# Kernel tuning notes

Measured on AMD Instinct MI355X. Metric: run time of the kernel, lower is better.

## Reference

```python
import jax, jax.numpy as jnp
import numpy as np

N_USERS, N_ITEMS = 40000, 60000
N = N_USERS + N_ITEMS
N_EDGES = 600000
IN_DIM, HID, OUT = 128, 256, 256


def setup_inputs() -> dict:
    key = jax.random.key(0)
    ks = jax.random.split(key, 8)
    return {
        "user_feat": jax.random.normal(ks[0], (N_USERS, IN_DIM), jnp.float32),
        "item_feat": jax.random.normal(ks[1], (N_ITEMS, IN_DIM), jnp.float32),
        "edge_rows": jax.random.randint(ks[2], (N_EDGES,), 0, N, jnp.int32),
        "edge_cols": jax.random.randint(ks[3], (N_EDGES,), 0, N, jnp.int32),
        "edge_vals": jax.random.uniform(ks[4], (N_EDGES,), jnp.float32),
        "W0": jax.random.normal(ks[5], (IN_DIM, HID), jnp.float32) * (1.0 / np.sqrt(IN_DIM)),
        "b0": jnp.zeros((HID,), jnp.float32),
        "Wres0": jax.random.normal(ks[6], (IN_DIM, HID), jnp.float32) * (1.0 / np.sqrt(IN_DIM)),
        "W1": jax.random.normal(ks[7], (HID, OUT), jnp.float32) * (1.0 / np.sqrt(HID)),
        "b1": jnp.zeros((OUT,), jnp.float32),
    }


def reference(user_feat, item_feat, edge_rows, edge_cols, edge_vals, W0, b0, Wres0, W1, b1):
    n_users = user_feat.shape[0]
    n_total = n_users + item_feat.shape[0]

    def spmm(x):  # sparse adjacency @ dense features via gather + segment-sum
        return jax.ops.segment_sum(edge_vals[:, None] * x[edge_cols], edge_rows,
                                   num_segments=n_total)

    # Layer 0: fc -> SpMM -> linear residual -> relu (norm=None, dropout eval no-op)
    x = jnp.concatenate([user_feat @ W0 + b0, item_feat @ W0 + b0])  # [N, HID]
    h = spmm(x)
    res = jnp.concatenate([user_feat, item_feat]) @ Wres0  # in_dim != out_dim -> Linear residual
    h = jax.nn.relu(h + res)

    # Layer 1 (last, encoding=False): fc -> SpMM, no residual/norm/activation
    x = h @ W1 + b1
    h = spmm(x)

    return h[:n_users], h[n_users:]
```

## Files before the change

### kernel.cpp

```cpp
#include <hip/hip_runtime.h>

#define N_USERS 40000
#define N_ITEMS 60000
#define N_TOTAL 100000
#define M_PAD   100032
#define NEDGES  600000
#define IN_DIM  128
#define HID     256

typedef short  bf16x8 __attribute__((ext_vector_type(8)));
typedef float  f32x4  __attribute__((ext_vector_type(4)));
typedef unsigned short ushort4v __attribute__((ext_vector_type(4)));
typedef unsigned short ushort8v __attribute__((ext_vector_type(8)));

__device__ __forceinline__ unsigned short f2bf(float f) {
    unsigned u = __builtin_bit_cast(unsigned, f);
    unsigned r = (u + 0x7FFFu + ((u >> 16) & 1u)) >> 16;
    return (unsigned short)r;
}
__device__ __forceinline__ float bf2f(unsigned short b) {
    unsigned u = ((unsigned)b) << 16;
    return __builtin_bit_cast(float, u);
}

__device__ __forceinline__ void gload_lds16(const void* g, void* l) {
    __builtin_amdgcn_global_load_lds(
        (const __attribute__((address_space(1))) unsigned int*)g,
        (__attribute__((address_space(3))) unsigned int*)l, 16, 0, 0);
}

__global__ __launch_bounds__(256) void prep_feats(const float* __restrict__ uf,
                                                  const float* __restrict__ itf,
                                                  unsigned short* __restrict__ outp) {
    const long i8 = (long)(blockIdx.x * 256 + threadIdx.x) * 8;
    if (i8 >= (long)N_TOTAL * IN_DIM) return;
    const long uend = (long)N_USERS * IN_DIM;
    const float4* src = (i8 < uend) ? (const float4*)(uf + i8)
                                    : (const float4*)(itf + (i8 - uend));
    float4 a = src[0], b = src[1];
    ushort8v o;
    o[0] = f2bf(a.x); o[1] = f2bf(a.y); o[2] = f2bf(a.z); o[3] = f2bf(a.w);
    o[4] = f2bf(b.x); o[5] = f2bf(b.y); o[6] = f2bf(b.z); o[7] = f2bf(b.w);
    *(ushort8v*)(outp + i8) = o;
}

__global__ __launch_bounds__(256) void prep_weights(const float* __restrict__ W0,
                                                    const float* __restrict__ Wres0,
                                                    const float* __restrict__ W1,
                                                    unsigned short* __restrict__ Wcat_t,
                                                    unsigned short* __restrict__ W1_t) {
    const int id = blockIdx.x * 256 + threadIdx.x;
    if (id < 512 * IN_DIM) {
        const int n = id >> 7, k = id & 127;
        const float v = (n < HID) ? W0[(size_t)k * HID + n]
                                  : Wres0[(size_t)k * HID + (n - HID)];
        Wcat_t[id] = f2bf(v);
    } else {
        const int id2 = id - 512 * IN_DIM;
        const int n = id2 >> 8, k = id2 & 255;
        W1_t[id2] = f2bf(W1[(size_t)k * HID + n]);
    }
}

template <int K>
__device__ __forceinline__ void stageB(const unsigned short* __restrict__ Bg,
                                       char* bs, int kk, int t) {
    #pragma unroll
    for (int i = 0; i < 4; ++i) {
        const int L = (i * 256 + t) * 16;
        const int n = L >> 6;
        const int q = (L >> 4) & 3;
        gload_lds16((const char*)(Bg + (size_t)n * K + kk + q * 8), bs + L);
    }
}

template <int K, int EPI>
__global__ __launch_bounds__(256) void mfma_gemm2(const unsigned short* __restrict__ A,
                                                  const unsigned short* __restrict__ Bt,
                                                  const float* __restrict__ bias,
                                                  unsigned short* __restrict__ out0,
                                                  unsigned short* __restrict__ out1) {
    constexpr int NK    = K / 32;
    constexpr int SHIFT = (K == 256) ? 9 : 8;
    __shared__ unsigned short As[64 * K];
    __shared__ unsigned short Bs[2][256 * 32];

    const int t  = threadIdx.x;
    const int w  = t >> 6, l = t & 63;
    const int fr = l & 15, fb = l >> 4;
    const int wr = w >> 1, wc = w & 1;
    const int m0 = blockIdx.x * 64;
    const int gy = blockIdx.y;

    const char* Ag = (const char*)(A + (size_t)m0 * K);
    constexpr int ACALLS = (64 * K * 2) / (16 * 256);
    #pragma unroll
    for (int i = 0; i < ACALLS; ++i) {
        const int L = (i * 256 + t) * 16;
        const int U = L ^ (((L >> SHIFT) & 7) << 4);
        gload_lds16(Ag + U, (char*)As + L);
    }
    const unsigned short* Bg = Bt + (size_t)gy * 256 * K;
    stageB<K>(Bg, (char*)Bs[0], 0, t);
    __syncthreads();

    f32x4 acc[2][8] = {};
    for (int kt = 0; kt < NK; ++kt) {
        if (kt + 1 < NK) stageB<K>(Bg, (char*)Bs[(kt + 1) & 1], (kt + 1) * 32, t);

        const char* as_base = (const char*)As;
        const char* bs_base = (const char*)Bs[kt & 1];
        bf16x8 af[2];
        #pragma unroll
        for (int rb = 0; rb < 2; ++rb) {
            const int row = wr * 32 + rb * 16 + fr;
            const int Sa = ((row * K + kt * 32 + fb * 8) * 2) ^ ((fr & 7) << 4);
            af[rb] = *(const bf16x8*)(as_base + Sa);
        }
        #pragma unroll
        for (int nt = 0; nt < 8; ++nt) {
            const int Sb = ((wc * 128 + nt * 16 + fr) * 32 + fb * 8) * 2;
            const bf16x8 bfr = *(const bf16x8*)(bs_base + Sb);
            acc[0][nt] = __builtin_amdgcn_mfma_f32_16x16x32_bf16(af[0], bfr, acc[0][nt], 0, 0, 0);
            acc[1][nt] = __builtin_amdgcn_mfma_f32_16x16x32_bf16(af[1], bfr, acc[1][nt], 0, 0, 0);
        }
        __syncthreads();
    }

    const bool use1 = (EPI == 1) && (gy == 1);
    unsigned short* outp = use1 ? out1 : out0;
    #pragma unroll
    for (int rb = 0; rb < 2; ++rb) {
        #pragma unroll
        for (int nt = 0; nt < 8; ++nt) {
            const int col = wc * 128 + nt * 16 + fr;
            const float bv = use1 ? 0.f : bias[col];
            #pragma unroll
            for (int j = 0; j < 4; ++j) {
                const int row = m0 + wr * 32 + rb * 16 + fb * 4 + j;
                if (row < N_TOTAL)
                    outp[(size_t)row * HID + col] = f2bf(acc[rb][nt][j] + bv);
            }
        }
    }
}

__global__ __launch_bounds__(256) void edge_histogram(const int* __restrict__ rows,
                                                      int* __restrict__ cnt) {
    int e = blockIdx.x * 256 + threadIdx.x;
    if (e < NEDGES) atomicAdd(&cnt[rows[e]], 1);
}

#define SCAN_B 1024
__global__ __launch_bounds__(SCAN_B) void scan_blocks(const int* __restrict__ cnt,
                                                      int* __restrict__ row_ptr,
                                                      int* __restrict__ bsums) {
    __shared__ int s[SCAN_B];
    const int gid = blockIdx.x * SCAN_B + threadIdx.x;
    const int v = (gid < N_TOTAL) ? cnt[gid] : 0;
    s[threadIdx.x] = v;
    __syncthreads();
    for (int off = 1; off < SCAN_B; off <<= 1) {
        int tv = (threadIdx.x >= off) ? s[threadIdx.x - off] : 0;
        __syncthreads();
        s[threadIdx.x] += tv;
        __syncthreads();
    }
    if (gid < N_TOTAL) row_ptr[gid] = s[threadIdx.x] - v;
    if (threadIdx.x == SCAN_B - 1) bsums[blockIdx.x] = s[threadIdx.x];
}

__global__ __launch_bounds__(128) void scan_sums(int* __restrict__ bsums, int nb) {
    __shared__ int s[128];
    const int v = (threadIdx.x < nb) ? bsums[threadIdx.x] : 0;
    s[threadIdx.x] = v;
    __syncthreads();
    for (int off = 1; off < 128; off <<= 1) {
        int tv = (threadIdx.x >= off) ? s[threadIdx.x - off] : 0;
        __syncthreads();
        s[threadIdx.x] += tv;
        __syncthreads();
    }
    if (threadIdx.x < nb) bsums[threadIdx.x] = s[threadIdx.x] - v;
}

__global__ __launch_bounds__(SCAN_B) void scan_apply(int* __restrict__ row_ptr,
                                                     const int* __restrict__ bsums,
                                                     int* __restrict__ next) {
    const int gid = blockIdx.x * SCAN_B + threadIdx.x;
    if (gid < N_TOTAL) {
        const int p = row_ptr[gid] + bsums[blockIdx.x];
        row_ptr[gid] = p;
        next[gid] = p;
    }
    if (gid == 0) row_ptr[N_TOTAL] = NEDGES;
}

__global__ __launch_bounds__(256) void csr_fill(const int* __restrict__ rows,
                                                const int* __restrict__ cols,
                                                const float* __restrict__ vals,
                                                int* __restrict__ next,
                                                int2* __restrict__ cvp) {
    int e = blockIdx.x * 256 + threadIdx.x;
    if (e >= NEDGES) return;
    const int slot = atomicAdd(&next[rows[e]], 1);
    int2 p;
    p.x = cols[e];
    p.y = __builtin_bit_cast(int, vals[e]);
    cvp[slot] = p;
}

template <bool FUSE>
__global__ __launch_bounds__(256) void spmm_bf16(const int* __restrict__ row_ptr,
                                                 const int2* __restrict__ cvp,
                                                 const unsigned short* __restrict__ X,
                                                 unsigned short* __restrict__ Ybf,
                                                 float* __restrict__ Yf) {
    const int wid  = (blockIdx.x * 256 + threadIdx.x) >> 6;
    const int lane = threadIdx.x & 63;
    if (wid >= N_TOTAL) return;
    const int beg = row_ptr[wid], end = row_ptr[wid + 1];

    float a0 = 0.f, a1 = 0.f, a2 = 0.f, a3 = 0.f;
    int e = beg;
    for (; e + 1 < end; e += 2) {
        const int2 p0 = cvp[e], p1 = cvp[e + 1];
        const float v0 = __builtin_bit_cast(float, p0.y);
        const float v1 = __builtin_bit_cast(float, p1.y);
        const ushort4v x0 = *(const ushort4v*)(X + (size_t)p0.x * HID + lane * 4);
        const ushort4v x1 = *(const ushort4v*)(X + (size_t)p1.x * HID + lane * 4);
        a0 = fmaf(v0, bf2f(x0[0]), a0); a1 = fmaf(v0, bf2f(x0[1]), a1);
        a2 = fmaf(v0, bf2f(x0[2]), a2); a3 = fmaf(v0, bf2f(x0[3]), a3);
        a0 = fmaf(v1, bf2f(x1[0]), a0); a1 = fmaf(v1, bf2f(x1[1]), a1);
        a2 = fmaf(v1, bf2f(x1[2]), a2); a3 = fmaf(v1, bf2f(x1[3]), a3);
    }
    if (e < end) {
        const int2 p0 = cvp[e];
        const float v0 = __builtin_bit_cast(float, p0.y);
        const ushort4v x0 = *(const ushort4v*)(X + (size_t)p0.x * HID + lane * 4);
        a0 = fmaf(v0, bf2f(x0[0]), a0); a1 = fmaf(v0, bf2f(x0[1]), a1);
        a2 = fmaf(v0, bf2f(x0[2]), a2); a3 = fmaf(v0, bf2f(x0[3]), a3);
    }

    if (FUSE) {
        unsigned short* yp = Ybf + (size_t)wid * HID + lane * 4;
        const ushort4v rv = *(const ushort4v*)yp;
        a0 = fmaxf(a0 + bf2f(rv[0]), 0.f);
        a1 = fmaxf(a1 + bf2f(rv[1]), 0.f);
        a2 = fmaxf(a2 + bf2f(rv[2]), 0.f);
        a3 = fmaxf(a3 + bf2f(rv[3]), 0.f);
        ushort4v o; o[0] = f2bf(a0); o[1] = f2bf(a1); o[2] = f2bf(a2); o[3] = f2bf(a3);
        *(ushort4v*)yp = o;
    } else {
        f32x4 o = {a0, a1, a2, a3};
        *(f32x4*)(Yf + (size_t)wid * HID + lane * 4) = o;
    }
}

extern "C" void kernel_launch(void* const* d_in, const int* in_sizes, int n_in,
                              void* d_out, int out_size, void* d_ws, size_t ws_size,
                              hipStream_t stream) {
    const float* user_feat = (const float*)d_in[0];
    const float* item_feat = (const float*)d_in[1];
    const int*   edge_rows = (const int*)d_in[2];
    const int*   edge_cols = (const int*)d_in[3];
    const float* edge_vals = (const float*)d_in[4];
    const float* W0    = (const float*)d_in[5];
    const float* b0    = (const float*)d_in[6];
    const float* Wres0 = (const float*)d_in[7];
    const float* W1    = (const float*)d_in[8];
    const float* b1    = (const float*)d_in[9];
    float* out = (float*)d_out;

    char* ws = (char*)d_ws;
    auto take = [&](size_t bytes) { char* p = ws; ws += (bytes + 255) & ~(size_t)255; return p; };
    unsigned short* x      = (unsigned short*)take((size_t)M_PAD * HID * 2);
    unsigned short* h      = (unsigned short*)take((size_t)M_PAD * HID * 2);
    unsigned short* feats  = (unsigned short*)take((size_t)M_PAD * IN_DIM * 2);
    unsigned short* Wcat_t = (unsigned short*)take(512 * IN_DIM * 2);
    unsigned short* W1_t   = (unsigned short*)take(HID * HID * 2);
    int*   row_ptr = (int*)take((N_TOTAL + 1) * 4);
    int*   cnt     = (int*)take(N_TOTAL * 4);
    int*   nxt     = (int*)take(N_TOTAL * 4);
    int*   bsums   = (int*)take(128 * 4);
    int2*  cvp     = (int2*)take((size_t)NEDGES * 8);

    const dim3 blk(256);
    const int nscan = (N_TOTAL + SCAN_B - 1) / SCAN_B;

    prep_feats<<<(N_TOTAL * IN_DIM / 8 + 255) / 256, blk, 0, stream>>>(user_feat, item_feat, feats);
    prep_weights<<<(512 * IN_DIM + HID * HID) / 256, blk, 0, stream>>>(W0, Wres0, W1, Wcat_t, W1_t);

    hipMemsetAsync(cnt, 0, N_TOTAL * 4, stream);
    edge_histogram<<<(NEDGES + 255) / 256, blk, 0, stream>>>(edge_rows, cnt);
    scan_blocks<<<nscan, SCAN_B, 0, stream>>>(cnt, row_ptr, bsums);
    scan_sums<<<1, 128, 0, stream>>>(bsums, nscan);
    scan_apply<<<nscan, SCAN_B, 0, stream>>>(row_ptr, bsums, nxt);
    csr_fill<<<(NEDGES + 255) / 256, blk, 0, stream>>>(edge_rows, edge_cols, edge_vals,
                                                       nxt, cvp);

    mfma_gemm2<IN_DIM, 1><<<dim3(M_PAD / 64, 2), blk, 0, stream>>>(feats, Wcat_t, b0, x, h);

    const int spmm_blocks = (N_TOTAL * 64 + 255) / 256;
    spmm_bf16<true><<<spmm_blocks, blk, 0, stream>>>(row_ptr, cvp, x, h, nullptr);

    mfma_gemm2<HID, 0><<<dim3(M_PAD / 64, 1), blk, 0, stream>>>(h, W1_t, b1, x, nullptr);

    spmm_bf16<false><<<spmm_blocks, blk, 0, stream>>>(row_ptr, cvp, x, nullptr, out);
}
```

Before: 458.5 us.

## Reassociate layer-0 SpMM before the fc and fuse the residual into one GEMM

Uses A(XW0+b0) = (AX)W0 + rowsum(A)·b0, so the first SpMM aggregates the 128-wide bf16 input features instead of the 256-wide hidden ones. It also returns per-row weight sums. A single K=256 GEMM over the concatenated [AX, X] against stacked [W0; Wres0] then computes the hidden layer, adds the scaled bias and applies ReLU in its epilogue. This removes the separate residual read-modify-write pass. The GEMM epilogue now stages its tile in LDS so it can write coalesced 16-byte global stores. The cost is an extra LDS round trip and a barrier per block, plus some extra rounding from storing AX in bf16.

Measured after the change: 422.0 us. 1.09x faster.

```diff
diff --git a/kernel.cpp b/kernel.cpp
--- a/kernel.cpp
+++ b/kernel.cpp
@@ -47,79 +47,84 @@
 __global__ __launch_bounds__(256) void prep_weights(const float* __restrict__ W0,
                                                     const float* __restrict__ Wres0,
                                                     const float* __restrict__ W1,
-                                                    unsigned short* __restrict__ Wcat_t,
+                                                    unsigned short* __restrict__ Wcat2_t,
                                                     unsigned short* __restrict__ W1_t) {
     const int id = blockIdx.x * 256 + threadIdx.x;
-    if (id < 512 * IN_DIM) {
-        const int n = id >> 7, k = id & 127;
-        const float v = (n < HID) ? W0[(size_t)k * HID + n]
-                                  : Wres0[(size_t)k * HID + (n - HID)];
-        Wcat_t[id] = f2bf(v);
+    if (id < HID * HID) {
+        const int n = id >> 8, k = id & 255;
+        const float v = (k < IN_DIM) ? W0[(size_t)k * HID + n]
+                                     : Wres0[(size_t)(k - IN_DIM) * HID + n];
+        Wcat2_t[id] = f2bf(v);
     } else {
-        const int id2 = id - 512 * IN_DIM;
+        const int id2 = id - HID * HID;
         const int n = id2 >> 8, k = id2 & 255;
         W1_t[id2] = f2bf(W1[(size_t)k * HID + n]);
     }
 }
 
-template <int K>
-__device__ __forceinline__ void stageB(const unsigned short* __restrict__ Bg,
-                                       char* bs, int kk, int t) {
+template <int EPI, bool DUAL>
+__global__ __launch_bounds__(256) void mfma_gemm4(const unsigned short* __restrict__ A0,
+                                                  const unsigned short* __restrict__ A1,
+                                                  const unsigned short* __restrict__ Bt,
+                                                  const float* __restrict__ bias,
+                                                  const float* __restrict__ dscale,
+                                                  unsigned short* __restrict__ outp) {
+    __shared__ unsigned short As[64 * 256];
+    __shared__ unsigned short Bs[2][256 * 32];
+
+    const int t  = threadIdx.x;
+    const int w  = t >> 6, l = t & 63;
+    const int fr = l & 15, fb = l >> 4;
+    const int wr = w >> 1, wc = w & 1;
+    const int m0 = blockIdx.x * 64;
+
+    #pragma unroll
+    for (int i = 0; i < 8; ++i) {
+        const int L   = (i * 256 + t) * 16;
+        const int row = L >> 9;
+        const int W   = L & 511;
+        const int U   = W ^ ((row & 7) << 4);
+        const char* src;
+        if (DUAL) {
+            src = (U < 256) ? (const char*)A0 + (size_t)(m0 + row) * 256 + U
+                            : (const char*)A1 + (size_t)(m0 + row) * 256 + (U - 256);
+        } else {
+            src = (const char*)A0 + (size_t)(m0 + row) * 512 + U;
+        }
+        gload_lds16(src, (char*)As + L);
+    }
     #pragma unroll
     for (int i = 0; i < 4; ++i) {
         const int L = (i * 256 + t) * 16;
         const int n = L >> 6;
         const int q = (L >> 4) & 3;
-        gload_lds16((const char*)(Bg + (size_t)n * K + kk + q * 8), bs + L);
-    }
-}
-
-template <int K, int EPI>
-__global__ __launch_bounds__(256) void mfma_gemm2(const unsigned short* __restrict__ A,
-                                                  const unsigned short* __restrict__ Bt,
-                                                  const float* __restrict__ bias,
-                                                  unsigned short* __restrict__ out0,
-                                                  unsigned short* __restrict__ out1) {
-    constexpr int NK    = K / 32;
-    constexpr int SHIFT = (K == 256) ? 9 : 8;
-    __shared__ unsigned short As[64 * K];
-    __shared__ unsigned short Bs[2][256 * 32];
-
-    const int t  = threadIdx.x;
-    const int w  = t >> 6, l = t & 63;
-    const int fr = l & 15, fb = l >> 4;
-    const int wr = w >> 1, wc = w & 1;
-    const int m0 = blockIdx.x * 64;
-    const int gy = blockIdx.y;
-
-    const char* Ag = (const char*)(A + (size_t)m0 * K);
-    constexpr int ACALLS = (64 * K * 2) / (16 * 256);
-    #pragma unroll
-    for (int i = 0; i < ACALLS; ++i) {
-        const int L = (i * 256 + t) * 16;
-        const int U = L ^ (((L >> SHIFT) & 7) << 4);
-        gload_lds16(Ag + U, (char*)As + L);
-    }
-    const unsigned short* Bg = Bt + (size_t)gy * 256 * K;
-    stageB<K>(Bg, (char*)Bs[0], 0, t);
+        gload_lds16((const char*)Bt + (size_t)n * 512 + q * 16, (char*)Bs[0] + L);
+    }
     __syncthreads();
 
     f32x4 acc[2][8] = {};
-    for (int kt = 0; kt < NK; ++kt) {
-        if (kt + 1 < NK) stageB<K>(Bg, (char*)Bs[(kt + 1) & 1], (kt + 1) * 32, t);
-
-        const char* as_base = (const char*)As;
-        const char* bs_base = (const char*)Bs[kt & 1];
+    for (int kt = 0; kt < 8; ++kt) {
+        if (kt < 7) {
+            #pragma unroll
+            for (int i = 0; i < 4; ++i) {
+                const int L = (i * 256 + t) * 16;
+                const int n = L >> 6;
+                const int q = (L >> 4) & 3;
+                gload_lds16((const char*)Bt + (size_t)n * 512 + (kt + 1) * 64 + q * 16,
+                            (char*)Bs[(kt + 1) & 1] + L);
+            }
+        }
         bf16x8 af[2];
         #pragma unroll
         for (int rb = 0; rb < 2; ++rb) {
             const int row = wr * 32 + rb * 16 + fr;
-            const int Sa = ((row * K + kt * 32 + fb * 8) * 2) ^ ((fr & 7) << 4);
-            af[rb] = *(const bf16x8*)(as_base + Sa);
-        }
+            const int Sa  = (row * 512 + kt * 64 + fb * 16) ^ ((fr & 7) << 4);
+            af[rb] = *(const bf16x8*)((const char*)As + Sa);
+        }
+        const char* bs_base = (const char*)Bs[kt & 1];
         #pragma unroll
         for (int nt = 0; nt < 8; ++nt) {
-            const int Sb = ((wc * 128 + nt * 16 + fr) * 32 + fb * 8) * 2;
+            const int Sb = (wc * 128 + nt * 16 + fr) * 64 + fb * 16;
             const bf16x8 bfr = *(const bf16x8*)(bs_base + Sb);
             acc[0][nt] = __builtin_amdgcn_mfma_f32_16x16x32_bf16(af[0], bfr, acc[0][nt], 0, 0, 0);
             acc[1][nt] = __builtin_amdgcn_mfma_f32_16x16x32_bf16(af[1], bfr, acc[1][nt], 0, 0, 0);
@@ -127,22 +132,30 @@
         __syncthreads();
     }
 
-    const bool use1 = (EPI == 1) && (gy == 1);
-    unsigned short* outp = use1 ? out1 : out0;
+    unsigned short* Hb = As;
     #pragma unroll
     for (int rb = 0; rb < 2; ++rb) {
         #pragma unroll
-        for (int nt = 0; nt < 8; ++nt) {
-            const int col = wc * 128 + nt * 16 + fr;
-            const float bv = use1 ? 0.f : bias[col];
+        for (int j = 0; j < 4; ++j) {
+            const int rl = wr * 32 + rb * 16 + fb * 4 + j;
+            const float ds = (EPI == 1) ? dscale[m0 + rl] : 0.f;
             #pragma unroll
-            for (int j = 0; j < 4; ++j) {
-                const int row = m0 + wr * 32 + rb * 16 + fb * 4 + j;
-                if (row < N_TOTAL)
-                    outp[(size_t)row * HID + col] = f2bf(acc[rb][nt][j] + bv);
+            for (int nt = 0; nt < 8; ++nt) {
+                const int col = wc * 128 + nt * 16 + fr;
+                float v = acc[rb][nt][j];
+                if (EPI == 1) v = fmaxf(v + ds * bias[col], 0.f);
+                else          v = v + bias[col];
+                Hb[rl * 256 + col] = f2bf(v);
             }
         }
     }
+    __syncthreads();
+    const int rowl = t >> 2;
+    const int cb   = (t & 3) * 64;
+    unsigned short* gp = outp + (size_t)(m0 + rowl) * HID + cb;
+    #pragma unroll
+    for (int i = 0; i < 8; ++i)
+        *(ushort8v*)(gp + i * 8) = *(const ushort8v*)(Hb + rowl * 256 + cb + i * 8);
 }
 
 __global__ __launch_bounds__(256) void edge_histogram(const int* __restrict__ rows,
@@ -210,12 +223,47 @@
     cvp[slot] = p;
 }
 
-template <bool FUSE>
-__global__ __launch_bounds__(256) void spmm_bf16(const int* __restrict__ row_ptr,
+__global__ __launch_bounds__(256) void spmm_feat(const int* __restrict__ row_ptr,
                                                  const int2* __restrict__ cvp,
-                                                 const unsigned short* __restrict__ X,
-                                                 unsigned short* __restrict__ Ybf,
-                                                 float* __restrict__ Yf) {
+                                                 const unsigned short* __restrict__ F,
+                                                 unsigned short* __restrict__ G,
+                                                 float* __restrict__ D) {
+    const int wid  = (blockIdx.x * 256 + threadIdx.x) >> 6;
+    const int lane = threadIdx.x & 63;
+    if (wid >= N_TOTAL) return;
+    const int beg = row_ptr[wid], end = row_ptr[wid + 1];
+
+    float a0 = 0.f, a1 = 0.f, ds = 0.f;
+    int e = beg;
+    for (; e + 1 < end; e += 2) {
+        const int2 p0 = cvp[e], p1 = cvp[e + 1];
+        const float v0 = __builtin_bit_cast(float, p0.y);
+        const float v1 = __builtin_bit_cast(float, p1.y);
+        ds += v0 + v1;
+        const unsigned x0 = *(const unsigned*)(F + (size_t)p0.x * IN_DIM + lane * 2);
+        const unsigned x1 = *(const unsigned*)(F + (size_t)p1.x * IN_DIM + lane * 2);
+        a0 = fmaf(v0, bf2f((unsigned short)(x0 & 0xFFFF)), a0);
+        a1 = fmaf(v0, bf2f((unsigned short)(x0 >> 16)),   a1);
+        a0 = fmaf(v1, bf2f((unsigned short)(x1 & 0xFFFF)), a0);
+        a1 = fmaf(v1, bf2f((unsigned short)(x1 >> 16)),   a1);
+    }
+    if (e < end) {
+        const int2 p0 = cvp[e];
+        const float v0 = __builtin_bit_cast(float, p0.y);
+        ds += v0;
+        const unsigned x0 = *(const unsigned*)(F + (size_t)p0.x * IN_DIM + lane * 2);
+        a0 = fmaf(v0, bf2f((unsigned short)(x0 & 0xFFFF)), a0);
+        a1 = fmaf(v0, bf2f((unsigned short)(x0 >> 16)),   a1);
+    }
+    const unsigned ov = (unsigned)f2bf(a0) | ((unsigned)f2bf(a1) << 16);
+    *(unsigned*)(G + (size_t)wid * IN_DIM + lane * 2) = ov;
+    if (lane == 0) D[wid] = ds;
+}
+
+__global__ __launch_bounds__(256) void spmm_out(const int* __restrict__ row_ptr,
+                                                const int2* __restrict__ cvp,
+                                                const unsigned short* __restrict__ X,
+                                                float* __restrict__ Yf) {
     const int wid  = (blockIdx.x * 256 + threadIdx.x) >> 6;
     const int lane = threadIdx.x & 63;
     if (wid >= N_TOTAL) return;
@@ -241,20 +289,8 @@
         a0 = fmaf(v0, bf2f(x0[0]), a0); a1 = fmaf(v0, bf2f(x0[1]), a1);
         a2 = fmaf(v0, bf2f(x0[2]), a2); a3 = fmaf(v0, bf2f(x0[3]), a3);
     }
-
-    if (FUSE) {
-        unsigned short* yp = Ybf + (size_t)wid * HID + lane * 4;
-        const ushort4v rv = *(const ushort4v*)yp;
-        a0 = fmaxf(a0 + bf2f(rv[0]), 0.f);
-        a1 = fmaxf(a1 + bf2f(rv[1]), 0.f);
-        a2 = fmaxf(a2 + bf2f(rv[2]), 0.f);
-        a3 = fmaxf(a3 + bf2f(rv[3]), 0.f);
-        ushort4v o; o[0] = f2bf(a0); o[1] = f2bf(a1); o[2] = f2bf(a2); o[3] = f2bf(a3);
-        *(ushort4v*)yp = o;
-    } else {
-        f32x4 o = {a0, a1, a2, a3};
-        *(f32x4*)(Yf + (size_t)wid * HID + lane * 4) = o;
-    }
+    f32x4 o = {a0, a1, a2, a3};
+    *(f32x4*)(Yf + (size_t)wid * HID + lane * 4) = o;
 }
 
 extern "C" void kernel_launch(void* const* d_in, const int* in_sizes, int n_in,
@@ -274,11 +310,13 @@
 
     char* ws = (char*)d_ws;
     auto take = [&](size_t bytes) { char* p = ws; ws += (bytes + 255) & ~(size_t)255; return p; };
-    unsigned short* x      = (unsigned short*)take((size_t)M_PAD * HID * 2);
-    unsigned short* h      = (unsigned short*)take((size_t)M_PAD * HID * 2);
-    unsigned short* feats  = (unsigned short*)take((size_t)M_PAD * IN_DIM * 2);
-    unsigned short* Wcat_t = (unsigned short*)take(512 * IN_DIM * 2);
-    unsigned short* W1_t   = (unsigned short*)take(HID * HID * 2);
+    unsigned short* feats   = (unsigned short*)take((size_t)M_PAD * IN_DIM * 2);
+    unsigned short* g       = (unsigned short*)take((size_t)M_PAD * IN_DIM * 2);
+    unsigned short* h       = (unsigned short*)take((size_t)M_PAD * HID * 2);
+    unsigned short* x2      = (unsigned short*)take((size_t)M_PAD * HID * 2);
+    float*          d       = (float*)take((size_t)M_PAD * 4);
+    unsigned short* Wcat2_t = (unsigned short*)take(HID * HID * 2);
+    unsigned short* W1_t    = (unsigned short*)take(HID * HID * 2);
     int*   row_ptr = (int*)take((N_TOTAL + 1) * 4);
     int*   cnt     = (int*)take(N_TOTAL * 4);
     int*   nxt     = (int*)take(N_TOTAL * 4);
@@ -289,7 +327,7 @@
     const int nscan = (N_TOTAL + SCAN_B - 1) / SCAN_B;
 
     prep_feats<<<(N_TOTAL * IN_DIM / 8 + 255) / 256, blk, 0, stream>>>(user_feat, item_feat, feats);
-    prep_weights<<<(512 * IN_DIM + HID * HID) / 256, blk, 0, stream>>>(W0, Wres0, W1, Wcat_t, W1_t);
+    prep_weights<<<(2 * HID * HID) / 256, blk, 0, stream>>>(W0, Wres0, W1, Wcat2_t, W1_t);
 
     hipMemsetAsync(cnt, 0, N_TOTAL * 4, stream);
     edge_histogram<<<(NEDGES + 255) / 256, blk, 0, stream>>>(edge_rows, cnt);
@@ -299,12 +337,13 @@
     csr_fill<<<(NEDGES + 255) / 256, blk, 0, stream>>>(edge_rows, edge_cols, edge_vals,
                                                        nxt, cvp);
 
-    mfma_gemm2<IN_DIM, 1><<<dim3(M_PAD / 64, 2), blk, 0, stream>>>(feats, Wcat_t, b0, x, h);
-
     const int spmm_blocks = (N_TOTAL * 64 + 255) / 256;
-    spmm_bf16<true><<<spmm_blocks, blk, 0, stream>>>(row_ptr, cvp, x, h, nullptr);
-
-    mfma_gemm2<HID, 0><<<dim3(M_PAD / 64, 1), blk, 0, stream>>>(h, W1_t, b1, x, nullptr);
-
-    spmm_bf16<false><<<spmm_blocks, blk, 0, stream>>>(row_ptr, cvp, x, nullptr, out);
-}
+
+    spmm_feat<<<spmm_blocks, blk, 0, stream>>>(row_ptr, cvp, feats, g, d);
+
+    mfma_gemm4<1, true><<<M_PAD / 64, blk, 0, stream>>>(g, feats, Wcat2_t, b0, d, h);
+
+    mfma_gemm4<0, false><<<M_PAD / 64, blk, 0, stream>>>(h, nullptr, W1_t, b1, nullptr, x2);
+
+    spmm_out<<<spmm_blocks, blk, 0, stream>>>(row_ptr, cvp, x2, out);
+}
```
